# Kernel tuning notes

Hardware: AMD Instinct MI355X
Metric: run time of the kernel (lower is better)

The kernel has to match this reference:

```python
import jax, jax.numpy as jnp
import numpy as np

H, D, Kd, Vd = 16, 1024, 64, 64
N, Mlen = 4096, 4096


def setup_inputs() -> dict:
    key = jax.random.key(0)
    ks = jax.random.split(key, 7)
    X = jax.random.normal(ks[0], (N, D), dtype=jnp.float32)
    M = jax.random.normal(ks[1], (Mlen, D), dtype=jnp.float32)
    mask = jax.random.randint(ks[2], (N, Mlen), 0, 2, dtype=jnp.int32)
    Wq = jax.random.normal(ks[3], (H, D, Kd), dtype=jnp.float32)
    Wk = jax.random.normal(ks[4], (H, D, Kd), dtype=jnp.float32)
    Wv = jax.random.normal(ks[5], (H, D, Vd), dtype=jnp.float32)
    Wo = jax.random.normal(ks[6], (H, Vd, D), dtype=jnp.float32)
    return {"X": X, "M": M, "mask": mask, "Wq": Wq, "Wk": Wk, "Wv": Wv, "Wo": Wo}


def reference(X, M, mask, Wq, Wk, Wv, Wo):
    # Projections: [h,n,k], [h,m,k], [h,m,v]
    Q = jnp.einsum('nd,hdk->hnk', X, Wq)
    K = jnp.einsum('md,hdk->hmk', M, Wk)
    V = jnp.einsum('md,hdv->hmv', M, Wv)
    # Masked attention (no scaling, matching the source)
    logits = jnp.einsum('hnk,hmk->hnm', Q, K)
    logits = jnp.where(mask[None, :, :] == 0, -jnp.inf, logits)
    weights = jax.nn.softmax(logits, axis=-1)
    O = jnp.einsum('hnm,hmv->hnv', weights, V)
    Y = jnp.einsum('hnv,hvd->nd', O, Wo)
    return Y
```

## Files before the change

kernel.cpp:

```cpp
#include <hip/hip_runtime.h>

typedef _Float16 half8 __attribute__((ext_vector_type(8)));
typedef _Float16 half4 __attribute__((ext_vector_type(4)));
typedef __fp16 fp16x2 __attribute__((ext_vector_type(2)));
typedef short short8 __attribute__((ext_vector_type(8)));
typedef short short4v __attribute__((ext_vector_type(4)));
typedef float floatx4 __attribute__((ext_vector_type(4)));

#define LOG2E 1.4426950408889634f

#define GLDS16(g, l) __builtin_amdgcn_global_load_lds( \
    (const __attribute__((address_space(1))) unsigned int*)(g), \
    (__attribute__((address_space(3))) unsigned int*)(l), 16, 0, 0)

static __device__ __forceinline__ short f2bf(float f){
  union { float f; unsigned u; } v; v.f = f;
  unsigned r = v.u + 0x7fffu + ((v.u >> 16) & 1u);
  return (short)(r >> 16);
}
static __device__ __forceinline__ float bf2f(short s){
  union { unsigned u; float f; } v; v.u = ((unsigned)(unsigned short)s) << 16;
  return v.f;
}

__global__ __launch_bounds__(256) void kconvA(const float* __restrict__ X,
                                              const float* __restrict__ Mm,
                                              short* __restrict__ XFh, short* __restrict__ XFl,
                                              short* __restrict__ MFh, short* __restrict__ MFl){
  int b = blockIdx.x;
  int t = threadIdx.x, w = t >> 6, l = t & 63, quad = l >> 4;
  int srcsel = b >> 8, ntile = b & 255;
  const float* A = srcsel ? Mm : X;
  short* oh = srcsel ? MFh : XFh;
  short* ol = srcsel ? MFl : XFl;
  int row = ntile*16 + (l & 15);
  #pragma unroll
  for (int i = 0; i < 8; i++){
    int kt = w*8 + i;
    const float* p = A + (size_t)row*1024 + kt*32 + quad*8;
    float4 v0 = *(const float4*)p, v1 = *(const float4*)(p + 4);
    float vv[8] = {v0.x,v0.y,v0.z,v0.w,v1.x,v1.y,v1.z,v1.w};
    short8 hh, ll;
    #pragma unroll
    for (int j = 0; j < 8; j++){
      short hb = f2bf(vv[j]); hh[j] = hb; ll[j] = f2bf(vv[j] - bf2f(hb));
    }
    size_t off = ((size_t)kt*256 + ntile)*512 + l*8;
    *(short8*)&oh[off] = hh;
    *(short8*)&ol[off] = ll;
  }
}

__global__ __launch_bounds__(256) void kconvW2(const float* __restrict__ Wq,
                                               const float* __restrict__ Wk,
                                               const float* __restrict__ Wv,
                                               short* __restrict__ WFh, short* __restrict__ WFl){
  __shared__ float T[128][68];
  int bidx = blockIdx.x, g = blockIdx.y;
  int mat = bidx >> 4, h = bidx & 15;
  const float* W = (mat == 0 ? Wq : (mat == 1 ? Wk : Wv)) + (size_t)h*65536;
  int t = threadIdx.x, w = t >> 6, l = t & 63, quad = (l >> 4) & 3, fl = l & 15;
  #pragma unroll
  for (int p = 0; p < 32; p++){
    int idx = p*256 + t, row = idx >> 6, col = idx & 63;
    T[row][col] = W[(size_t)(g*128 + row)*64 + col];
  }
  __syncthreads();
  for (int ktl = 0; ktl < 4; ktl++){
    short8 hh, ll;
    #pragma unroll
    for (int j = 0; j < 8; j++){
      float v = T[ktl*32 + quad*8 + j][w*16 + fl];
      short hb = f2bf(v); hh[j] = hb; ll[j] = f2bf(v - bf2f(hb));
    }
    size_t frag = ((size_t)bidx*32 + g*4 + ktl)*4 + w;
    *(short8*)&WFh[frag*512 + l*8] = hh;
    *(short8*)&WFl[frag*512 + l*8] = ll;
  }
}

__global__ __launch_bounds__(256) void kmaskpack(const int* __restrict__ mask,
                                                 unsigned* __restrict__ bits){
  int w = blockIdx.x * 256 + threadIdx.x;
  const int* p = mask + (size_t)w * 32;
  unsigned b = 0;
  #pragma unroll
  for (int i = 0; i < 32; i++) b |= (p[i] != 0) ? (1u << i) : 0u;
  bits[w] = b;
}

__global__ __launch_bounds__(256) void ktransw(const float* __restrict__ src,
                                               short* __restrict__ dsth,
                                               short* __restrict__ dstl,
                                               int R, int C){
  __shared__ float tile[32][33];
  size_t boff = (size_t)blockIdx.z * R * C;
  src += boff; dsth += boff; dstl += boff;
  int r0 = blockIdx.y*32, c0 = blockIdx.x*32;
  int t = threadIdx.x, tr = t >> 3, tc = (t & 7)*4;
  const float* s = src + (size_t)(r0 + tr)*C + c0 + tc;
  #pragma unroll
  for (int i = 0; i < 4; i++) tile[tr][tc + i] = s[i];
  __syncthreads();
  short* dh = dsth + (size_t)(c0 + tr)*R + r0 + tc;
  short* dl = dstl + (size_t)(c0 + tr)*R + r0 + tc;
  #pragma unroll
  for (int i = 0; i < 4; i++){
    float v = tile[tc + i][tr];
    short hb = f2bf(v);
    dh[i] = hb; dl[i] = f2bf(v - bf2f(hb));
  }
}

__global__ __launch_bounds__(256,2) void kproj2(
    const short* __restrict__ XFh, const short* __restrict__ XFl,
    const short* __restrict__ MFh, const short* __restrict__ MFl,
    const short* __restrict__ WFh, const short* __restrict__ WFl,
    _Float16* __restrict__ QFh, _Float16* __restrict__ QFl,
    _Float16* __restrict__ KFh, _Float16* __restrict__ KFl,
    _Float16* __restrict__ VF)
{
  __shared__ short AhL[4096], AlL[4096], BhL[2048], BlL[2048];
  int cb = blockIdx.x, rb = blockIdx.y;
  int mat = cb >> 4, h = cb & 15;
  const short* Ah = (mat == 0) ? XFh : MFh;
  const short* Al = (mat == 0) ? XFl : MFl;
  int t = threadIdx.x, w = t >> 6, l = t & 63, quad = l >> 4, ln = l & 15;
  floatx4 acc[2][4] = {};
  for (int kt = 0; kt < 32; kt++){
    __syncthreads();
    size_t abase = ((size_t)kt*256 + rb*8)*512;
    #pragma unroll
    for (int i = 0; i < 2; i++){
      int cidx = i*256 + t;
      GLDS16(Ah + abase + cidx*8, &AhL[(i*256 + w*64)*8]);
      GLDS16(Al + abase + cidx*8, &AlL[(i*256 + w*64)*8]);
    }
    size_t bbase = (((size_t)cb*32 + kt)*4)*512;
    GLDS16(WFh + bbase + t*8, &BhL[(w*64)*8]);
    GLDS16(WFl + bbase + t*8, &BlL[(w*64)*8]);
    __syncthreads();
    short8 bh[4], bl[4];
    #pragma unroll
    for (int nt = 0; nt < 4; nt++){
      bh[nt] = *(short8*)&BhL[nt*512 + l*8];
      bl[nt] = *(short8*)&BlL[nt*512 + l*8];
    }
    #pragma unroll
    for (int mt = 0; mt < 2; mt++){
      short8 ah = *(short8*)&AhL[(w*2 + mt)*512 + l*8];
      short8 al = *(short8*)&AlL[(w*2 + mt)*512 + l*8];
      #pragma unroll
      for (int nt = 0; nt < 4; nt++){
        acc[mt][nt] = __builtin_amdgcn_mfma_f32_16x16x32_bf16(ah, bh[nt], acc[mt][nt], 0, 0, 0);
        acc[mt][nt] = __builtin_amdgcn_mfma_f32_16x16x32_bf16(ah, bl[nt], acc[mt][nt], 0, 0, 0);
        acc[mt][nt] = __builtin_amdgcn_mfma_f32_16x16x32_bf16(al, bh[nt], acc[mt][nt], 0, 0, 0);
      }
    }
  }
  int row0 = rb*128;
  if (mat == 2){
    #pragma unroll
    for (int mt = 0; mt < 2; mt++)
      #pragma unroll
      for (int nt = 0; nt < 4; nt++){
        union { fp16x2 h2[2]; unsigned u2[2]; } pu;
        pu.h2[0] = __builtin_amdgcn_cvt_pkrtz(acc[mt][nt][0], acc[mt][nt][1]);
        pu.h2[1] = __builtin_amdgcn_cvt_pkrtz(acc[mt][nt][2], acc[mt][nt][3]);
        size_t base = (((size_t)h*32 + rb)*16 + nt*4 + w)*512;
        *(uint2*)&VF[base + (quad*16 + ln)*8 + mt*4] = *(uint2*)&pu.u2[0];
      }
  } else {
    #pragma unroll
    for (int mt = 0; mt < 2; mt++)
      #pragma unroll
      for (int nt = 0; nt < 4; nt++)
        #pragma unroll
        for (int rg = 0; rg < 4; rg++){
          int n = row0 + w*32 + mt*16 + quad*4 + rg;
          int c = nt*16 + ln;
          float v = acc[mt][nt][rg];
          if (mat == 0) v *= LOG2E;
          _Float16 hi = (_Float16)v;
          _Float16 lo = (_Float16)(v - (float)hi);
          int lane2 = (n & 15) + (((c >> 3) & 3) << 4);
          size_t off = (((size_t)h*256 + (n >> 4))*2 + (c >> 5))*512 + lane2*8 + (c & 7);
          if (mat == 0){ QFh[off] = hi; QFl[off] = lo; }
          else         { KFh[off] = hi; KFl[off] = lo; }
        }
  }
}

__global__ __launch_bounds__(256,3) void kattn5(
    const _Float16* __restrict__ QFh, const _Float16* __restrict__ QFl,
    const _Float16* __restrict__ KFh, const _Float16* __restrict__ KFl,
    const _Float16* __restrict__ VF, const unsigned* __restrict__ bits,
    short* __restrict__ Ows)
{
  __shared__ _Float16 KBh[8192], KBl[8192], VB[8192];
  int bx = blockIdx.x, h = bx & 15, qb = bx >> 4, q0 = qb*128;
  int t = threadIdx.x, w = t >> 6, l = t & 63, quad = l >> 4, ln = l & 15;

  half8 qh[2][2], ql[2][2];
  #pragma unroll
  for (int nt2 = 0; nt2 < 2; nt2++)
    #pragma unroll
    for (int kc = 0; kc < 2; kc++){
      size_t off = (((size_t)h*256 + qb*8 + w*2 + nt2)*2 + kc)*512 + l*8;
      qh[nt2][kc] = *(const half8*)&QFh[off];
      ql[nt2][kc] = *(const half8*)&QFl[off];
    }

  floatx4 o[2][4] = {};
  float mst[2] = {-1e30f, -1e30f}, lst[2] = {0.f, 0.f};

  for (int kt = 0; kt < 32; kt++){
    __syncthreads();
    size_t kb = (size_t)h*262144 + (size_t)kt*8192;
    #pragma unroll
    for (int i = 0; i < 4; i++){
      int cidx = i*256 + t;
      GLDS16(KFh + kb + cidx*8, &KBh[(i*256 + w*64)*8]);
      GLDS16(KFl + kb + cidx*8, &KBl[(i*256 + w*64)*8]);
      GLDS16(VF  + kb + cidx*8, &VB [(i*256 + w*64)*8]);
    }
    uint4 mw[2];
    mw[0] = *(const uint4*)&bits[(size_t)(q0 + w*32 + ln)*128 + kt*4];
    mw[1] = *(const uint4*)&bits[(size_t)(q0 + w*32 + 16 + ln)*128 + kt*4];
    __syncthreads();

    floatx4 st[2][8] = {};
    #pragma unroll
    for (int kc = 0; kc < 2; kc++)
      #pragma unroll
      for (int m8 = 0; m8 < 8; m8++){
        half8 kh = *(half8*)&KBh[(m8*2 + kc)*512 + l*8];
        half8 kl = *(half8*)&KBl[(m8*2 + kc)*512 + l*8];
        #pragma unroll
        for (int nt2 = 0; nt2 < 2; nt2++){
          st[nt2][m8] = __builtin_amdgcn_mfma_f32_16x16x32_f16(kh, qh[nt2][kc], st[nt2][m8], 0, 0, 0);
          st[nt2][m8] = __builtin_amdgcn_mfma_f32_16x16x32_f16(kl, qh[nt2][kc], st[nt2][m8], 0, 0, 0);
          st[nt2][m8] = __builtin_amdgcn_mfma_f32_16x16x32_f16(kh, ql[nt2][kc], st[nt2][m8], 0, 0, 0);
        }
      }

    #pragma unroll
    for (int nt2 = 0; nt2 < 2; nt2++){
      const unsigned* mwp = (const unsigned*)&mw[nt2];
      #pragma unroll
      for (int m8 = 0; m8 < 8; m8++){
        unsigned nib = (mwp[m8 >> 1] >> ((m8 & 1)*16 + quad*4)) & 15u;
        #pragma unroll
        for (int rg = 0; rg < 4; rg++)
          if (!((nib >> rg) & 1u)) st[nt2][m8][rg] = -1e30f;
      }
      float mx = st[nt2][0][0];
      #pragma unroll
      for (int m8 = 0; m8 < 8; m8++)
        #pragma unroll
        for (int rg = 0; rg < 4; rg++) mx = fmaxf(mx, st[nt2][m8][rg]);
      mx = fmaxf(mx, __shfl_xor(mx, 16));
      mx = fmaxf(mx, __shfl_xor(mx, 32));
      float mnew = fmaxf(mst[nt2], mx);
      float alpha = exp2f(mst[nt2] - mnew);
      mst[nt2] = mnew;
      lst[nt2] *= alpha;
      #pragma unroll
      for (int vt = 0; vt < 4; vt++) o[nt2][vt] *= alpha;
      float ssum = 0.f;
      #pragma unroll
      for (int m8 = 0; m8 < 8; m8++)
        #pragma unroll
        for (int rg = 0; rg < 4; rg++){
          float p = exp2f(st[nt2][m8][rg] - mnew);
          st[nt2][m8][rg] = p; ssum += p;
        }
      ssum += __shfl_xor(ssum, 16);
      ssum += __shfl_xor(ssum, 32);
      lst[nt2] += ssum;
    }

    #pragma unroll
    for (int p = 0; p < 4; p++){
      half8 vfp[4];
      #pragma unroll
      for (int vt = 0; vt < 4; vt++)
        vfp[vt] = *(half8*)&VB[(vt*4 + p)*512 + l*8];
      #pragma unroll
      for (int nt2 = 0; nt2 < 2; nt2++)
        #pragma unroll
        for (int sub = 0; sub < 2; sub++){
          int m8 = p*2 + sub;
          union { fp16x2 h2[2]; half4 h4; } pu;
          pu.h2[0] = __builtin_amdgcn_cvt_pkrtz(st[nt2][m8][0], st[nt2][m8][1]);
          pu.h2[1] = __builtin_amdgcn_cvt_pkrtz(st[nt2][m8][2], st[nt2][m8][3]);
          #pragma unroll
          for (int vt = 0; vt < 4; vt++){
            half4 va = sub ? __builtin_shufflevector(vfp[vt], vfp[vt], 4,5,6,7)
                           : __builtin_shufflevector(vfp[vt], vfp[vt], 0,1,2,3);
            o[nt2][vt] = __builtin_amdgcn_mfma_f32_16x16x16f16(va, pu.h4, o[nt2][vt], 0, 0, 0);
          }
        }
    }
  }

  #pragma unroll
  for (int nt2 = 0; nt2 < 2; nt2++){
    float li = lst[nt2];
    float inv = (li > 0.f) ? (1.f / li) : 0.f;
    int n = q0 + w*32 + nt2*16 + ln;
    #pragma unroll
    for (int vt = 0; vt < 4; vt++){
      short4v pk;
      #pragma unroll
      for (int rg = 0; rg < 4; rg++) pk[rg] = f2bf(o[nt2][vt][rg]*inv);
      *(short4v*)&Ows[(size_t)n*1024 + h*64 + vt*16 + quad*4] = pk;
    }
  }
}

__global__ __launch_bounds__(256,2) void kfinal(const short* __restrict__ Ain,
                                                const short* __restrict__ Bt,
                                                float* __restrict__ Y)
{
  __shared__ short Al[128*48];
  __shared__ short Bl[64*48];
  int cb = blockIdx.x, rb = blockIdx.y;
  int row0 = rb*128, col0 = cb*64;
  int t = threadIdx.x, w = t >> 6, l = t & 63, quad = l >> 4, ln = l & 15;
  floatx4 acc[2][4] = {};
  for (int d0 = 0; d0 < 1024; d0 += 32){
    #pragma unroll
    for (int i = 0; i < 2; i++){
      int u = t + i*256, r = u >> 2, s = u & 3;
      *(int4*)&Al[r*48 + s*8] = *(const int4*)&Ain[(size_t)(row0 + r)*1024 + d0 + s*8];
    }
    { int r = t >> 2, s = t & 3;
      *(int4*)&Bl[r*48 + s*8] = *(const int4*)&Bt[(size_t)(col0 + r)*1024 + d0 + s*8]; }
    __syncthreads();
    short8 bf[4];
    #pragma unroll
    for (int nt = 0; nt < 4; nt++) bf[nt] = *(short8*)&Bl[(nt*16 + ln)*48 + quad*8];
    #pragma unroll
    for (int mt = 0; mt < 2; mt++){
      short8 af = *(short8*)&Al[(w*32 + mt*16 + ln)*48 + quad*8];
      #pragma unroll
      for (int nt = 0; nt < 4; nt++)
        acc[mt][nt] = __builtin_amdgcn_mfma_f32_16x16x32_bf16(af, bf[nt], acc[mt][nt], 0, 0, 0);
    }
    __syncthreads();
  }
  #pragma unroll
  for (int mt = 0; mt < 2; mt++)
    #pragma unroll
    for (int nt = 0; nt < 4; nt++)
      #pragma unroll
      for (int rg = 0; rg < 4; rg++){
        int n = row0 + w*32 + mt*16 + quad*4 + rg;
        int c = col0 + nt*16 + ln;
        Y[(size_t)n*1024 + c] = acc[mt][nt][rg];
      }
}

extern "C" void kernel_launch(void* const* d_in, const int* in_sizes, int n_in,
                              void* d_out, int out_size, void* d_ws, size_t ws_size,
                              hipStream_t stream){
  (void)in_sizes; (void)n_in; (void)out_size; (void)ws_size;
  const float* X    = (const float*)d_in[0];
  const float* Mm   = (const float*)d_in[1];
  const int*   mask = (const int*)d_in[2];
  const float* Wq   = (const float*)d_in[3];
  const float* Wk   = (const float*)d_in[4];
  const float* Wv   = (const float*)d_in[5];
  const float* Wo   = (const float*)d_in[6];
  float* Y = (float*)d_out;
  char* ws = (char*)d_ws;
  const size_t MB = 1024*1024;
  short*    XFh   = (short*)   (ws +  0*MB);
  short*    XFl   = (short*)   (ws +  8*MB);
  short*    MFh   = (short*)   (ws + 16*MB);
  short*    MFl   = (short*)   (ws + 24*MB);
  short*    WFh   = (short*)   (ws + 32*MB);
  short*    WFl   = (short*)   (ws + 38*MB);
  unsigned* bits  = (unsigned*)(ws + 44*MB);
  _Float16* QFh   = (_Float16*)(ws + 46*MB);
  _Float16* QFl   = (_Float16*)(ws + 54*MB);
  _Float16* KFh   = (_Float16*)(ws + 62*MB);
  _Float16* KFl   = (_Float16*)(ws + 70*MB);
  _Float16* VF    = (_Float16*)(ws + 78*MB);
  short*    Ows   = (short*)   (ws +  0*MB);
  short*    Wot   = (short*)   (ws +  8*MB);
  short*    Wotl  = (short*)   (ws + 10*MB);

  kconvA<<<512, 256, 0, stream>>>(X, Mm, XFh, XFl, MFh, MFl);
  kconvW2<<<dim3(48,8), 256, 0, stream>>>(Wq, Wk, Wv, WFh, WFl);
  kmaskpack<<<2048, 256, 0, stream>>>(mask, bits);
  kproj2<<<dim3(48,32), 256, 0, stream>>>(XFh, XFl, MFh, MFl, WFh, WFl,
                                          QFh, QFl, KFh, KFl, VF);
  ktransw<<<dim3(32,32,1), 256, 0, stream>>>(Wo, Wot, Wotl, 1024, 1024);
  kattn5<<<512, 256, 0, stream>>>(QFh, QFl, KFh, KFl, VF, bits, Ows);
  kfinal<<<dim3(16,32), 256, 0, stream>>>(Ows, Wot, Y);
}
```

Measured before the change: 507.1 us.

## Halve attention tile sizes to double grid and raise occupancy

The attention kernel now gives each block 64 queries and a 64-key tile instead of 128 queries and 128 keys. The grid doubles to 1024 blocks, shared memory per block halves, and the launch bound rises to 4 blocks per CU. V loads are re-indexed to fetch half of the original 128-key V tile layout each iteration. The aim is better CU fill and latency hiding with fewer registers, at the cost of twice as many K/V loads per query and twice as many barrier iterations.

```diff
diff --git a/kernel.cpp b/kernel.cpp
--- a/kernel.cpp
+++ b/kernel.cpp
@@ -191,129 +191,119 @@
   }
 }
 
-__global__ __launch_bounds__(256,3) void kattn5(
+__global__ __launch_bounds__(256,4) void kattn6(
     const _Float16* __restrict__ QFh, const _Float16* __restrict__ QFl,
     const _Float16* __restrict__ KFh, const _Float16* __restrict__ KFl,
     const _Float16* __restrict__ VF, const unsigned* __restrict__ bits,
     short* __restrict__ Ows)
 {
-  __shared__ _Float16 KBh[8192], KBl[8192], VB[8192];
-  int bx = blockIdx.x, h = bx & 15, qb = bx >> 4, q0 = qb*128;
+  __shared__ _Float16 KBh[4096], KBl[4096], VB[4096];
+  int bx = blockIdx.x, h = bx & 15, qb = bx >> 4, q0 = qb*64;
   int t = threadIdx.x, w = t >> 6, l = t & 63, quad = l >> 4, ln = l & 15;
 
-  half8 qh[2][2], ql[2][2];
-  #pragma unroll
-  for (int nt2 = 0; nt2 < 2; nt2++)
-    #pragma unroll
-    for (int kc = 0; kc < 2; kc++){
-      size_t off = (((size_t)h*256 + qb*8 + w*2 + nt2)*2 + kc)*512 + l*8;
-      qh[nt2][kc] = *(const half8*)&QFh[off];
-      ql[nt2][kc] = *(const half8*)&QFl[off];
-    }
-
-  floatx4 o[2][4] = {};
-  float mst[2] = {-1e30f, -1e30f}, lst[2] = {0.f, 0.f};
-
-  for (int kt = 0; kt < 32; kt++){
-    __syncthreads();
-    size_t kb = (size_t)h*262144 + (size_t)kt*8192;
-    #pragma unroll
-    for (int i = 0; i < 4; i++){
+  half8 qh[2], ql[2];
+  #pragma unroll
+  for (int kc = 0; kc < 2; kc++){
+    size_t off = (((size_t)h*256 + qb*4 + w)*2 + kc)*512 + l*8;
+    qh[kc] = *(const half8*)&QFh[off];
+    ql[kc] = *(const half8*)&QFl[off];
+  }
+
+  floatx4 o[4] = {};
+  float mst = -1e30f, lst = 0.f;
+
+  for (int kt = 0; kt < 64; kt++){
+    __syncthreads();
+    size_t kb = (size_t)h*262144 + (size_t)kt*4096;
+    size_t vb = (size_t)h*262144 + (size_t)(kt >> 1)*8192;
+    int vhalf = (kt & 1)*2;
+    #pragma unroll
+    for (int i = 0; i < 2; i++){
       int cidx = i*256 + t;
       GLDS16(KFh + kb + cidx*8, &KBh[(i*256 + w*64)*8]);
       GLDS16(KFl + kb + cidx*8, &KBl[(i*256 + w*64)*8]);
-      GLDS16(VF  + kb + cidx*8, &VB [(i*256 + w*64)*8]);
-    }
-    uint4 mw[2];
-    mw[0] = *(const uint4*)&bits[(size_t)(q0 + w*32 + ln)*128 + kt*4];
-    mw[1] = *(const uint4*)&bits[(size_t)(q0 + w*32 + 16 + ln)*128 + kt*4];
-    __syncthreads();
-
-    floatx4 st[2][8] = {};
+      int lu = cidx >> 6, uoff = (cidx & 63)*8;
+      int gu = (lu >> 1)*4 + vhalf + (lu & 1);
+      GLDS16(VF + vb + (size_t)gu*512 + uoff, &VB[(i*256 + w*64)*8]);
+    }
+    uint2 mwv = *(const uint2*)&bits[(size_t)(q0 + w*16 + ln)*128 + kt*2];
+    __syncthreads();
+
+    floatx4 st[4] = {};
     #pragma unroll
     for (int kc = 0; kc < 2; kc++)
       #pragma unroll
-      for (int m8 = 0; m8 < 8; m8++){
+      for (int m8 = 0; m8 < 4; m8++){
         half8 kh = *(half8*)&KBh[(m8*2 + kc)*512 + l*8];
         half8 kl = *(half8*)&KBl[(m8*2 + kc)*512 + l*8];
+        st[m8] = __builtin_amdgcn_mfma_f32_16x16x32_f16(kh, qh[kc], st[m8], 0, 0, 0);
+        st[m8] = __builtin_amdgcn_mfma_f32_16x16x32_f16(kl, qh[kc], st[m8], 0, 0, 0);
+        st[m8] = __builtin_amdgcn_mfma_f32_16x16x32_f16(kh, ql[kc], st[m8], 0, 0, 0);
+      }
+
+    const unsigned mwp[2] = {mwv.x, mwv.y};
+    #pragma unroll
+    for (int m8 = 0; m8 < 4; m8++){
+      unsigned nib = (mwp[m8 >> 1] >> ((m8 & 1)*16 + quad*4)) & 15u;
+      #pragma unroll
+      for (int rg = 0; rg < 4; rg++)
+        if (!((nib >> rg) & 1u)) st[m8][rg] = -1e30f;
+    }
+    float mx = st[0][0];
+    #pragma unroll
+    for (int m8 = 0; m8 < 4; m8++)
+      #pragma unroll
+      for (int rg = 0; rg < 4; rg++) mx = fmaxf(mx, st[m8][rg]);
+    mx = fmaxf(mx, __shfl_xor(mx, 16));
+    mx = fmaxf(mx, __shfl_xor(mx, 32));
+    float mnew = fmaxf(mst, mx);
+    float alpha = exp2f(mst - mnew);
+    mst = mnew;
+    lst *= alpha;
+    #pragma unroll
+    for (int vt = 0; vt < 4; vt++) o[vt] *= alpha;
+    float ssum = 0.f;
+    #pragma unroll
+    for (int m8 = 0; m8 < 4; m8++)
+      #pragma unroll
+      for (int rg = 0; rg < 4; rg++){
+        float p = exp2f(st[m8][rg] - mnew);
+        st[m8][rg] = p; ssum += p;
+      }
+    ssum += __shfl_xor(ssum, 16);
+    ssum += __shfl_xor(ssum, 32);
+    lst += ssum;
+
+    #pragma unroll
+    for (int p = 0; p < 2; p++){
+      half8 vfp[4];
+      #pragma unroll
+      for (int vt = 0; vt < 4; vt++)
+        vfp[vt] = *(half8*)&VB[((vt*2 + p)*512) + l*8];
+      #pragma unroll
+      for (int sub = 0; sub < 2; sub++){
+        int m8 = p*2 + sub;
+        union { fp16x2 h2[2]; half4 h4; } pu;
+        pu.h2[0] = __builtin_amdgcn_cvt_pkrtz(st[m8][0], st[m8][1]);
+        pu.h2[1] = __builtin_amdgcn_cvt_pkrtz(st[m8][2], st[m8][3]);
         #pragma unroll
-        for (int nt2 = 0; nt2 < 2; nt2++){
-          st[nt2][m8] = __builtin_amdgcn_mfma_f32_16x16x32_f16(kh, qh[nt2][kc], st[nt2][m8], 0, 0, 0);
-          st[nt2][m8] = __builtin_amdgcn_mfma_f32_16x16x32_f16(kl, qh[nt2][kc], st[nt2][m8], 0, 0, 0);
-          st[nt2][m8] = __builtin_amdgcn_mfma_f32_16x16x32_f16(kh, ql[nt2][kc], st[nt2][m8], 0, 0, 0);
+        for (int vt = 0; vt < 4; vt++){
+          half4 va = sub ? __builtin_shufflevector(vfp[vt], vfp[vt], 4,5,6,7)
+                         : __builtin_shufflevector(vfp[vt], vfp[vt], 0,1,2,3);
+          o[vt] = __builtin_amdgcn_mfma_f32_16x16x16f16(va, pu.h4, o[vt], 0, 0, 0);
         }
       }
-
-    #pragma unroll
-    for (int nt2 = 0; nt2 < 2; nt2++){
-      const unsigned* mwp = (const unsigned*)&mw[nt2];
-      #pragma unroll
-      for (int m8 = 0; m8 < 8; m8++){
-        unsigned nib = (mwp[m8 >> 1] >> ((m8 & 1)*16 + quad*4)) & 15u;
-        #pragma unroll
-        for (int rg = 0; rg < 4; rg++)
-          if (!((nib >> rg) & 1u)) st[nt2][m8][rg] = -1e30f;
-      }
-      float mx = st[nt2][0][0];
-      #pragma unroll
-      for (int m8 = 0; m8 < 8; m8++)
-        #pragma unroll
-        for (int rg = 0; rg < 4; rg++) mx = fmaxf(mx, st[nt2][m8][rg]);
-      mx = fmaxf(mx, __shfl_xor(mx, 16));
-      mx = fmaxf(mx, __shfl_xor(mx, 32));
-      float mnew = fmaxf(mst[nt2], mx);
-      float alpha = exp2f(mst[nt2] - mnew);
-      mst[nt2] = mnew;
-      lst[nt2] *= alpha;
-      #pragma unroll
-      for (int vt = 0; vt < 4; vt++) o[nt2][vt] *= alpha;
-      float ssum = 0.f;
-      #pragma unroll
-      for (int m8 = 0; m8 < 8; m8++)
-        #pragma unroll
-        for (int rg = 0; rg < 4; rg++){
-          float p = exp2f(st[nt2][m8][rg] - mnew);
-          st[nt2][m8][rg] = p; ssum += p;
-        }
-      ssum += __shfl_xor(ssum, 16);
-      ssum += __shfl_xor(ssum, 32);
-      lst[nt2] += ssum;
-    }
-
-    #pragma unroll
-    for (int p = 0; p < 4; p++){
-      half8 vfp[4];
-      #pragma unroll
-      for (int vt = 0; vt < 4; vt++)
-        vfp[vt] = *(half8*)&VB[(vt*4 + p)*512 + l*8];
-      #pragma unroll
-      for (int nt2 = 0; nt2 < 2; nt2++)
-        #pragma unroll
-        for (int sub = 0; sub < 2; sub++){
-          int m8 = p*2 + sub;
-          union { fp16x2 h2[2]; half4 h4; } pu;
-          pu.h2[0] = __builtin_amdgcn_cvt_pkrtz(st[nt2][m8][0], st[nt2][m8][1]);
-          pu.h2[1] = __builtin_amdgcn_cvt_pkrtz(st[nt2][m8][2], st[nt2][m8][3]);
-          #pragma unroll
-          for (int vt = 0; vt < 4; vt++){
-            half4 va = sub ? __builtin_shufflevector(vfp[vt], vfp[vt], 4,5,6,7)
-                           : __builtin_shufflevector(vfp[vt], vfp[vt], 0,1,2,3);
-            o[nt2][vt] = __builtin_amdgcn_mfma_f32_16x16x16f16(va, pu.h4, o[nt2][vt], 0, 0, 0);
-          }
-        }
-    }
-  }
-
-  #pragma unroll
-  for (int nt2 = 0; nt2 < 2; nt2++){
-    float li = lst[nt2];
-    float inv = (li > 0.f) ? (1.f / li) : 0.f;
-    int n = q0 + w*32 + nt2*16 + ln;
+    }
+  }
+
+  {
+    float inv = (lst > 0.f) ? (1.f / lst) : 0.f;
+    int n = q0 + w*16 + ln;
     #pragma unroll
     for (int vt = 0; vt < 4; vt++){
       short4v pk;
       #pragma unroll
-      for (int rg = 0; rg < 4; rg++) pk[rg] = f2bf(o[nt2][vt][rg]*inv);
+      for (int rg = 0; rg < 4; rg++) pk[rg] = f2bf(o[vt][rg]*inv);
       *(short4v*)&Ows[(size_t)n*1024 + h*64 + vt*16 + quad*4] = pk;
     }
   }
@@ -398,6 +388,6 @@
   kproj2<<<dim3(48,32), 256, 0, stream>>>(XFh, XFl, MFh, MFl, WFh, WFl,
                                           QFh, QFl, KFh, KFl, VF);
   ktransw<<<dim3(32,32,1), 256, 0, stream>>>(Wo, Wot, Wotl, 1024, 1024);
-  kattn5<<<512, 256, 0, stream>>>(QFh, QFl, KFh, KFl, VF, bits, Ows);
+  kattn6<<<1024, 256, 0, stream>>>(QFh, QFl, KFh, KFl, VF, bits, Ows);
   kfinal<<<dim3(16,32), 256, 0, stream>>>(Ows, Wot, Y);
 }
```

Result: faster. 493.6 us (-2.7%).
